# Kernel optimization log

Measured on AMD Instinct MI355X. Metric: run time of the kernel, lower is better.

The kernel has to match this reference:

```python
import jax, jax.numpy as jnp
import numpy as np

N_NODES = 100000
N_EDGES = 1600000
IN_CH = 48
OUT_CH = 64
K = 2


def setup_inputs() -> dict:
    key = jax.random.key(0)
    k1, k2, k3, k4 = jax.random.split(key, 4)
    x = jax.random.normal(k1, (N_NODES, IN_CH), dtype=jnp.float32)
    edge_index = jax.random.randint(k2, (2, N_EDGES), 0, N_NODES, dtype=jnp.int64)
    W = jax.random.normal(k3, (IN_CH, OUT_CH), dtype=jnp.float32) * (1.0 / np.sqrt(IN_CH))
    b = jax.random.normal(k4, (OUT_CH,), dtype=jnp.float32) * 0.01
    return {"x": x, "edge_index": edge_index, "W": W, "b": b}


def _propagate(x, row, col):
    n = x.shape[0]
    # degree of each node counted over col (destination) indices
    deg = jax.ops.segment_sum(jnp.ones_like(col, dtype=x.dtype), col, num_segments=n)
    deg_inv_sqrt = jnp.where(deg > 0, jax.lax.rsqrt(jnp.where(deg > 0, deg, 1.0)), 0.0)
    norm = deg_inv_sqrt[row] * deg_inv_sqrt[col]  # [E]
    # gather-scale-scatter: out[col] += x[row] * norm
    msgs = x[row] * norm[:, None]  # [E, d]
    return jax.ops.segment_sum(msgs, col, num_segments=n)


def reference(x, edge_index, W, b):
    row, col = edge_index[0], edge_index[1]
    h = x
    for _ in range(K):
        h = _propagate(h, row, col)
    return h @ W + b
```

## Files before the change

kernel.cpp:

```cpp
#include <hip/hip_runtime.h>
#include <hip/hip_bf16.h>
#include <hip/hip_fp16.h>


#define N_NODES 100000
#define N_EDGES 1600000
#define IN_CH 48
#define OUT_CH 64
#define NBUCKETS 392
#define CAP 4608
#define EPB 2048
#define EPR 8
#define NBLK_EDGE 782
#define NBLK_BKT 391
#define RSTRIDE 32

__global__ void init_kernel(int* __restrict__ bucketCursor, int* __restrict__ binTotal) {
    int t = threadIdx.x;
    if (t < NBUCKETS) bucketCursor[t] = t * CAP;
    if (t < 64) binTotal[t] = 0;
}

__global__ void bucket_scatter_kernel(const int* __restrict__ row, const int* __restrict__ col,
                                      int* __restrict__ bucketCursor, int* __restrict__ edge_packed) {
    __shared__ int lh[NBUCKETS];
    __shared__ int lofs[NBUCKETS];
    __shared__ int lbase[NBUCKETS];
    __shared__ int stage[EPB];
    __shared__ unsigned short sbkt[EPB];
    __shared__ int wsum[4];
    int tid = threadIdx.x;
    int base = blockIdx.x * EPB;
    for (int i = tid; i < NBUCKETS; i += 256) lh[i] = 0;
    __syncthreads();
    #pragma unroll
    for (int k = 0; k < EPR; k++) {
        int e = base + k * 256 + tid;
        if (e < N_EDGES) atomicAdd(&lh[col[e] >> 8], 1);
    }
    __syncthreads();
    {
        int c0 = (tid < 196) ? lh[2 * tid] : 0;
        int c1 = (tid < 196) ? lh[2 * tid + 1] : 0;
        int s = c0 + c1;
        int incl = s;
        int lane = tid & 63, w = tid >> 6;
        #pragma unroll
        for (int o = 1; o < 64; o <<= 1) {
            int v = __shfl_up(incl, o, 64);
            if (lane >= o) incl += v;
        }
        if (lane == 63) wsum[w] = incl;
        __syncthreads();
        int wbase = 0;
        for (int k = 0; k < w; k++) wbase += wsum[k];
        int ex = wbase + incl - s;
        if (tid < 196) {
            lofs[2 * tid]     = ex;
            lofs[2 * tid + 1] = ex + c0;
        }
    }
    __syncthreads();
    for (int i = tid; i < NBUCKETS; i += 256) {
        int c = lh[i];
        if (c > 0) lbase[i] = atomicAdd(&bucketCursor[i], c);
        lh[i] = 0;
    }
    __syncthreads();
    #pragma unroll
    for (int k = 0; k < EPR; k++) {
        int e = base + k * 256 + tid;
        if (e < N_EDGES) {
            int c = col[e];
            int bkt = c >> 8;
            int r = atomicAdd(&lh[bkt], 1);
            int slot = lofs[bkt] + r;
            stage[slot] = (row[e] << 8) | (c & 255);
            sbkt[slot] = (unsigned short)bkt;
        }
    }
    __syncthreads();
    int total = (base + EPB <= N_EDGES) ? EPB : (N_EDGES - base);
    for (int i = tid; i < total; i += 256) {
        int bkt = sbkt[i];
        int dst = lbase[bkt] + (i - lofs[bkt]);
        if (dst < (bkt + 1) * CAP)
            edge_packed[dst] = stage[i];
    }
}

__global__ void fine_sort_kernel(const int* __restrict__ edge_packed,
                                 const int* __restrict__ bucketCursor,
                                 int* __restrict__ edge_src,
                                 int* __restrict__ deg, int* __restrict__ start,
                                 float* __restrict__ dis, int* __restrict__ binTotal) {
    __shared__ int fh[256];
    __shared__ int cur[256];
    __shared__ int bh[64];
    __shared__ int wsum2[4];
    __shared__ int stage[CAP];
    int b = blockIdx.x;
    int t = threadIdx.x;
    int s0 = b * CAP;
    int s1 = min(bucketCursor[b], (b + 1) * CAP);
    int n_edges = s1 - s0;
    int nodeBase = b << 8;
    if (t < 256) fh[t] = 0;
    if (t < 64) bh[t] = 0;
    __syncthreads();
    for (int j = t; j < n_edges; j += 512) {
        int rc = edge_packed[s0 + j];
        stage[j] = rc;
        atomicAdd(&fh[rc & 255], 1);
    }
    __syncthreads();
    if (t < 256) {
        int c = fh[t];
        int incl = c;
        int sl = t & 63, sw = t >> 6;
        #pragma unroll
        for (int o = 1; o < 64; o <<= 1) {
            int v = __shfl_up(incl, o, 64);
            if (sl >= o) incl += v;
        }
        if (sl == 63) wsum2[sw] = incl;
        __syncthreads();
        int wbase = 0;
        for (int k = 0; k < sw; k++) wbase += wsum2[k];
        incl += wbase;
        int ex = incl - c;
        int node = nodeBase + t;
        bool valid = (node < N_NODES);
        int d = c;
        float dv = (valid && d > 0) ? rsqrtf((float)d) : 0.0f;
        cur[t] = ex;
        if (valid) {
            deg[node] = d;
            start[node] = s0 + ex;
            dis[node] = dv;
            atomicAdd(&bh[min(d, 63)], 1);
        }
    } else {
        __syncthreads();
    }
    __syncthreads();
    for (int j = t; j < n_edges; j += 512) {
        int rc = stage[j];
        int p = atomicAdd(&cur[rc & 255], 1);
        edge_src[s0 + p] = rc >> 8;
    }
    __syncthreads();
    if (t < 64 && bh[t]) atomicAdd(&binTotal[t], bh[t]);
}

__global__ void scale_kernel(const float* __restrict__ x, const float* __restrict__ dis,
                             __half2* __restrict__ xs) {
    int g = blockIdx.x * 32 + (threadIdx.x >> 3);
    int c = (threadIdx.x & 7) * 3;
    float dd = dis[g];
    const float2* px = (const float2*)x + g * 24 + c;
    float2 v0 = px[0], v1 = px[1], v2 = px[2];
    __half2* q = xs + g * RSTRIDE + c;
    q[0] = __floats2half2_rn(v0.x * dd, v0.y * dd);
    q[1] = __floats2half2_rn(v1.x * dd, v1.y * dd);
    q[2] = __floats2half2_rn(v2.x * dd, v2.y * dd);
}

__global__ void binscan_kernel(const int* __restrict__ binTotal, int* __restrict__ binCursor) {
    if (threadIdx.x == 0) {
        int s = 0;
        for (int k = 63; k >= 0; k--) { binCursor[k] = s; s += binTotal[k]; }
    }
}

__global__ void order_kernel(const int* __restrict__ deg, const int* __restrict__ start,
                             const float* __restrict__ dis, int* __restrict__ binCursor,
                             int4* __restrict__ nodeinfo, int n) {
    __shared__ int lhist[64];
    __shared__ int lbase[64];
    int i = blockIdx.x * 256 + threadIdx.x;
    if (threadIdx.x < 64) lhist[threadIdx.x] = 0;
    __syncthreads();
    int bin = 0, myrank = 0;
    if (i < n) {
        bin = min(deg[i], 63);
        myrank = atomicAdd(&lhist[bin], 1);
    }
    __syncthreads();
    if (threadIdx.x < 64 && lhist[threadIdx.x] > 0)
        lbase[threadIdx.x] = atomicAdd(&binCursor[threadIdx.x], lhist[threadIdx.x]);
    __syncthreads();
    if (i < n)
        nodeinfo[lbase[bin] + myrank] = make_int4(i, start[i], deg[i], __float_as_int(dis[i]));
}

#define LOAD3(p, v0, v1, v2) { v0 = (p)[0]; v1 = (p)[1]; v2 = (p)[2]; }
#define ACC6(v0, v1, v2) { \
    float2 u0 = __half22float2(v0), u1 = __half22float2(v1), u2 = __half22float2(v2); \
    a0 += u0.x; a1 += u0.y; a2 += u1.x; a3 += u1.y; a4 += u2.x; a5 += u2.y; }
#define ACC6B(v0, v1, v2) { \
    float2 u0 = __half22float2(v0), u1 = __half22float2(v1), u2 = __half22float2(v2); \
    b0 += u0.x; b1 += u0.y; b2 += u1.x; b3 += u1.y; b4 += u2.x; b5 += u2.y; }

#define DECLD(P) __half2 P##00,P##01,P##02,P##10,P##11,P##12,P##20,P##21,P##22,P##30,P##31,P##32
#define DECLS(S) int S##0, S##1, S##2, S##3
#define LOADSRC(S) { S##0 = edge_src[j]; S##1 = edge_src[j+1]; \
                     S##2 = edge_src[j+2]; S##3 = edge_src[j+3]; j += 4; }
#define ISSUED(P, S, basep) { \
    const __half2* q0 = basep + S##0 * RSTRIDE + lane3; \
    const __half2* q1 = basep + S##1 * RSTRIDE + lane3; \
    const __half2* q2 = basep + S##2 * RSTRIDE + lane3; \
    const __half2* q3 = basep + S##3 * RSTRIDE + lane3; \
    P##00 = q0[0]; P##01 = q0[1]; P##02 = q0[2]; \
    P##10 = q1[0]; P##11 = q1[1]; P##12 = q1[2]; \
    P##20 = q2[0]; P##21 = q2[1]; P##22 = q2[2]; \
    P##30 = q3[0]; P##31 = q3[1]; P##32 = q3[2]; }
#define CONSUMED(P) { ACC6(P##00,P##01,P##02); ACC6B(P##10,P##11,P##12); \
                      ACC6(P##20,P##21,P##22); ACC6B(P##30,P##31,P##32); }

#define GATHER_PIPELINE(basep) { \
    int m = (e - s) >> 2; \
    DECLD(A); DECLD(B); \
    DECLS(sa); DECLS(sb); \
    if (m >= 2) { \
        LOADSRC(sa); LOADSRC(sb); \
        ISSUED(A, sa, basep); \
        m -= 2; \
        while (m >= 2) { \
            LOADSRC(sa); \
            ISSUED(B, sb, basep); \
            CONSUMED(A); \
            LOADSRC(sb); \
            ISSUED(A, sa, basep); \
            CONSUMED(B); \
            m -= 2; \
        } \
        if (m == 1) { \
            LOADSRC(sa); \
            ISSUED(B, sb, basep); \
            CONSUMED(A); \
            ISSUED(A, sa, basep); \
            CONSUMED(B); \
            CONSUMED(A); \
        } else { \
            ISSUED(B, sb, basep); \
            CONSUMED(A); \
            CONSUMED(B); \
        } \
    } else if (m == 1) { \
        LOADSRC(sa); \
        ISSUED(A, sa, basep); \
        CONSUMED(A); \
    } \
    for (; j < e; ++j) { \
        const __half2* p0 = basep + edge_src[j] * RSTRIDE + lane3; \
        __half2 v00, v01, v02; \
        LOAD3(p0, v00, v01, v02); \
        ACC6(v00, v01, v02); \
    } \
    a0 += b0; a1 += b1; a2 += b2; a3 += b3; a4 += b4; a5 += b5; }

__global__ void gather1_kernel(const __half2* __restrict__ xs,
                               const int* __restrict__ edge_src,
                               const int4* __restrict__ nodeinfo,
                               __half2* __restrict__ h1) {
    int g = blockIdx.x * 32 + (threadIdx.x >> 3);
    int lane3 = (threadIdx.x & 7) * 3;
    int4 ni = nodeinfo[g];
    int node = ni.x, s = ni.y, e = s + ni.z;
    float dv = __int_as_float(ni.w);
    float a0 = 0, a1 = 0, a2 = 0, a3 = 0, a4 = 0, a5 = 0;
    float b0 = 0, b1 = 0, b2 = 0, b3 = 0, b4 = 0, b5 = 0;
    int j = s;
    GATHER_PIPELINE(xs);
    float sc = dv * dv;
    __half2* q = h1 + node * RSTRIDE + lane3;
    q[0] = __floats2half2_rn(a0 * sc, a1 * sc);
    q[1] = __floats2half2_rn(a2 * sc, a3 * sc);
    q[2] = __floats2half2_rn(a4 * sc, a5 * sc);
}

__global__ void gather2_gemm_kernel(const __half2* __restrict__ h1,
                                    const int* __restrict__ edge_src,
                                    const int4* __restrict__ nodeinfo,
                                    const float* __restrict__ W,
                                    const float* __restrict__ bias,
                                    float* __restrict__ out) {
    __shared__ float sW[IN_CH * OUT_CH];
    __shared__ float sb[OUT_CH];
    __shared__ float sh[32][IN_CH + 1];

    for (int i = threadIdx.x; i < IN_CH * OUT_CH; i += 256) sW[i] = W[i];
    if (threadIdx.x < OUT_CH) sb[threadIdx.x] = bias[threadIdx.x];

    int nl = threadIdx.x >> 3;
    int lane = threadIdx.x & 7;
    int lane3 = lane * 3;
    int g = blockIdx.x * 32 + nl;
    int4 ni = nodeinfo[g];
    int node = ni.x, s = ni.y, e = s + ni.z;
    float dv = __int_as_float(ni.w);

    float a0 = 0, a1 = 0, a2 = 0, a3 = 0, a4 = 0, a5 = 0;
    float b0 = 0, b1 = 0, b2 = 0, b3 = 0, b4 = 0, b5 = 0;
    int j = s;
    GATHER_PIPELINE(h1);
    int c0 = 6 * lane;
    sh[nl][c0 + 0] = a0 * dv;
    sh[nl][c0 + 1] = a1 * dv;
    sh[nl][c0 + 2] = a2 * dv;
    sh[nl][c0 + 3] = a3 * dv;
    sh[nl][c0 + 4] = a4 * dv;
    sh[nl][c0 + 5] = a5 * dv;
    __syncthreads();

    int j0 = lane * 8;
    float acc[8];
    #pragma unroll
    for (int i = 0; i < 8; i++) acc[i] = sb[j0 + i];
    for (int k = 0; k < IN_CH; k++) {
        float s0 = sh[nl][k];
        #pragma unroll
        for (int i = 0; i < 8; i++) acc[i] += s0 * sW[k * OUT_CH + j0 + i];
    }
    float4* o = (float4*)(out + (size_t)node * OUT_CH + j0);
    o[0] = make_float4(acc[0], acc[1], acc[2], acc[3]);
    o[1] = make_float4(acc[4], acc[5], acc[6], acc[7]);
}

extern "C" void kernel_launch(void* const* d_in, const int* in_sizes, int n_in,
                              void* d_out, int out_size, void* d_ws, size_t ws_size,
                              hipStream_t stream) {
    const float* x   = (const float*)d_in[0];
    const int*   ei  = (const int*)d_in[1];
    const float* W   = (const float*)d_in[2];
    const float* b   = (const float*)d_in[3];
    float* out = (float*)d_out;

    const int* row = ei;
    const int* col = ei + N_EDGES;

    int* ws_i = (int*)d_ws;
    int* bucketCursor = ws_i;
    int* binTotal     = ws_i + 512;
    int* binCursor    = ws_i + 576;
    int* deg          = ws_i + 1024;
    int* start        = ws_i + 101376;
    float* dis        = (float*)(ws_i + 201728);
    int4* nodeinfo    = (int4*)(ws_i + 302080);
    int* edge_packed  = ws_i + 703488;
    __half2* xs       = (__half2*)(ws_i + 703488);
    int* edge_src     = ws_i + 3903488;
    __half2* h1       = (__half2*)(ws_i + 5709824);

    init_kernel<<<1, 512, 0, stream>>>(bucketCursor, binTotal);
    bucket_scatter_kernel<<<NBLK_EDGE, 256, 0, stream>>>(row, col, bucketCursor, edge_packed);
    fine_sort_kernel<<<NBLK_BKT, 512, 0, stream>>>(edge_packed, bucketCursor,
                                                   edge_src, deg, start, dis, binTotal);
    scale_kernel<<<N_NODES / 32, 256, 0, stream>>>(x, dis, xs);
    binscan_kernel<<<1, 64, 0, stream>>>(binTotal, binCursor);
    order_kernel<<<(N_NODES + 255) / 256, 256, 0, stream>>>(deg, start, dis, binCursor,
                                                            nodeinfo, N_NODES);

    gather1_kernel<<<N_NODES / 32, 256, 0, stream>>>(xs, edge_src, nodeinfo, h1);
    gather2_gemm_kernel<<<N_NODES / 32, 256, 0, stream>>>(h1, edge_src, nodeinfo, W, b, out);
}
```

Before: 206.8 us.

## Drop init and binscan kernels, simplify bucket scatter with single pass

```diff
diff --git a/kernel.cpp b/kernel.cpp
--- a/kernel.cpp
+++ b/kernel.cpp
@@ -15,57 +15,15 @@
 #define NBLK_BKT 391
 #define RSTRIDE 32
 
-__global__ void init_kernel(int* __restrict__ bucketCursor, int* __restrict__ binTotal) {
-    int t = threadIdx.x;
-    if (t < NBUCKETS) bucketCursor[t] = t * CAP;
-    if (t < 64) binTotal[t] = 0;
-}
-
 __global__ void bucket_scatter_kernel(const int* __restrict__ row, const int* __restrict__ col,
-                                      int* __restrict__ bucketCursor, int* __restrict__ edge_packed) {
+                                      int* __restrict__ bucketCnt, int* __restrict__ edge_packed) {
     __shared__ int lh[NBUCKETS];
-    __shared__ int lofs[NBUCKETS];
     __shared__ int lbase[NBUCKETS];
-    __shared__ int stage[EPB];
+    __shared__ int rec[EPB];
     __shared__ unsigned short sbkt[EPB];
-    __shared__ int wsum[4];
     int tid = threadIdx.x;
     int base = blockIdx.x * EPB;
     for (int i = tid; i < NBUCKETS; i += 256) lh[i] = 0;
-    __syncthreads();
-    #pragma unroll
-    for (int k = 0; k < EPR; k++) {
-        int e = base + k * 256 + tid;
-        if (e < N_EDGES) atomicAdd(&lh[col[e] >> 8], 1);
-    }
-    __syncthreads();
-    {
-        int c0 = (tid < 196) ? lh[2 * tid] : 0;
-        int c1 = (tid < 196) ? lh[2 * tid + 1] : 0;
-        int s = c0 + c1;
-        int incl = s;
-        int lane = tid & 63, w = tid >> 6;
-        #pragma unroll
-        for (int o = 1; o < 64; o <<= 1) {
-            int v = __shfl_up(incl, o, 64);
-            if (lane >= o) incl += v;
-        }
-        if (lane == 63) wsum[w] = incl;
-        __syncthreads();
-        int wbase = 0;
-        for (int k = 0; k < w; k++) wbase += wsum[k];
-        int ex = wbase + incl - s;
-        if (tid < 196) {
-            lofs[2 * tid]     = ex;
-            lofs[2 * tid + 1] = ex + c0;
-        }
-    }
-    __syncthreads();
-    for (int i = tid; i < NBUCKETS; i += 256) {
-        int c = lh[i];
-        if (c > 0) lbase[i] = atomicAdd(&bucketCursor[i], c);
-        lh[i] = 0;
-    }
     __syncthreads();
     #pragma unroll
     for (int k = 0; k < EPR; k++) {
@@ -73,24 +31,30 @@
         if (e < N_EDGES) {
             int c = col[e];
             int bkt = c >> 8;
-            int r = atomicAdd(&lh[bkt], 1);
-            int slot = lofs[bkt] + r;
-            stage[slot] = (row[e] << 8) | (c & 255);
-            sbkt[slot] = (unsigned short)bkt;
+            rec[k * 256 + tid] = (row[e] << 8) | (c & 255);
+            sbkt[k * 256 + tid] = (unsigned short)bkt;
+            atomicAdd(&lh[bkt], 1);
         }
     }
     __syncthreads();
-    int total = (base + EPB <= N_EDGES) ? EPB : (N_EDGES - base);
+    for (int i = tid; i < NBUCKETS; i += 256) {
+        int c = lh[i];
+        if (c > 0) lbase[i] = i * CAP + atomicAdd(&bucketCnt[i], c);
+        lh[i] = 0;
+    }
+    __syncthreads();
+    int total = min(EPB, N_EDGES - base);
     for (int i = tid; i < total; i += 256) {
         int bkt = sbkt[i];
-        int dst = lbase[bkt] + (i - lofs[bkt]);
+        int p = atomicAdd(&lh[bkt], 1);
+        int dst = lbase[bkt] + p;
         if (dst < (bkt + 1) * CAP)
-            edge_packed[dst] = stage[i];
+            edge_packed[dst] = rec[i];
     }
 }
 
 __global__ void fine_sort_kernel(const int* __restrict__ edge_packed,
-                                 const int* __restrict__ bucketCursor,
+                                 const int* __restrict__ bucketCnt,
                                  int* __restrict__ edge_src,
                                  int* __restrict__ deg, int* __restrict__ start,
                                  float* __restrict__ dis, int* __restrict__ binTotal) {
@@ -102,8 +66,7 @@
     int b = blockIdx.x;
     int t = threadIdx.x;
     int s0 = b * CAP;
-    int s1 = min(bucketCursor[b], (b + 1) * CAP);
-    int n_edges = s1 - s0;
+    int n_edges = min(bucketCnt[b], CAP);
     int nodeBase = b << 8;
     if (t < 256) fh[t] = 0;
     if (t < 64) bh[t] = 0;
@@ -166,32 +129,41 @@
     q[2] = __floats2half2_rn(v2.x * dd, v2.y * dd);
 }
 
-__global__ void binscan_kernel(const int* __restrict__ binTotal, int* __restrict__ binCursor) {
-    if (threadIdx.x == 0) {
-        int s = 0;
-        for (int k = 63; k >= 0; k--) { binCursor[k] = s; s += binTotal[k]; }
-    }
-}
-
 __global__ void order_kernel(const int* __restrict__ deg, const int* __restrict__ start,
-                             const float* __restrict__ dis, int* __restrict__ binCursor,
+                             const float* __restrict__ dis,
+                             const int* __restrict__ binTotal, int* __restrict__ binCursor2,
                              int4* __restrict__ nodeinfo, int n) {
     __shared__ int lhist[64];
     __shared__ int lbase[64];
-    int i = blockIdx.x * 256 + threadIdx.x;
-    if (threadIdx.x < 64) lhist[threadIdx.x] = 0;
-    __syncthreads();
-    int bin = 0, myrank = 0;
+    int t = threadIdx.x;
+    int i = blockIdx.x * 256 + t;
+    if (t < 64) lhist[t] = 0;
+    __syncthreads();
+    int bin = 0, myrank = 0, d = 0;
+    float dv = 0.0f;
     if (i < n) {
-        bin = min(deg[i], 63);
+        d = deg[i];
+        dv = dis[i];
+        bin = min(d, 63);
         myrank = atomicAdd(&lhist[bin], 1);
     }
     __syncthreads();
-    if (threadIdx.x < 64 && lhist[threadIdx.x] > 0)
-        lbase[threadIdx.x] = atomicAdd(&binCursor[threadIdx.x], lhist[threadIdx.x]);
+    if (t < 64) {
+        int c = binTotal[t];
+        int incl = c;
+        #pragma unroll
+        for (int o = 1; o < 64; o <<= 1) {
+            int v = __shfl_up(incl, o, 64);
+            if (t >= o) incl += v;
+        }
+        int tot = __shfl(incl, 63, 64);
+        int S = tot - incl;
+        int add = (lhist[t] > 0) ? atomicAdd(&binCursor2[t], lhist[t]) : 0;
+        lbase[t] = S + add;
+    }
     __syncthreads();
     if (i < n)
-        nodeinfo[lbase[bin] + myrank] = make_int4(i, start[i], deg[i], __float_as_int(dis[i]));
+        nodeinfo[lbase[bin] + myrank] = make_int4(i, start[i], d, __float_as_int(dv));
 }
 
 #define LOAD3(p, v0, v1, v2) { v0 = (p)[0]; v1 = (p)[1]; v2 = (p)[2]; }
@@ -341,9 +313,9 @@
     const int* col = ei + N_EDGES;
 
     int* ws_i = (int*)d_ws;
-    int* bucketCursor = ws_i;
+    int* bucketCnt    = ws_i;
     int* binTotal     = ws_i + 512;
-    int* binCursor    = ws_i + 576;
+    int* binCursor2   = ws_i + 576;
     int* deg          = ws_i + 1024;
     int* start        = ws_i + 101376;
     float* dis        = (float*)(ws_i + 201728);
@@ -353,14 +325,14 @@
     int* edge_src     = ws_i + 3903488;
     __half2* h1       = (__half2*)(ws_i + 5709824);
 
-    init_kernel<<<1, 512, 0, stream>>>(bucketCursor, binTotal);
-    bucket_scatter_kernel<<<NBLK_EDGE, 256, 0, stream>>>(row, col, bucketCursor, edge_packed);
-    fine_sort_kernel<<<NBLK_BKT, 512, 0, stream>>>(edge_packed, bucketCursor,
+    hipMemsetAsync(d_ws, 0, 640 * sizeof(int), stream);
+
+    bucket_scatter_kernel<<<NBLK_EDGE, 256, 0, stream>>>(row, col, bucketCnt, edge_packed);
+    fine_sort_kernel<<<NBLK_BKT, 512, 0, stream>>>(edge_packed, bucketCnt,
                                                    edge_src, deg, start, dis, binTotal);
     scale_kernel<<<N_NODES / 32, 256, 0, stream>>>(x, dis, xs);
-    binscan_kernel<<<1, 64, 0, stream>>>(binTotal, binCursor);
-    order_kernel<<<(N_NODES + 255) / 256, 256, 0, stream>>>(deg, start, dis, binCursor,
-                                                            nodeinfo, N_NODES);
+    order_kernel<<<(N_NODES + 255) / 256, 256, 0, stream>>>(deg, start, dis, binTotal,
+                                                            binCursor2, nodeinfo, N_NODES);
 
     gather1_kernel<<<N_NODES / 32, 256, 0, stream>>>(xs, edge_src, nodeinfo, h1);
     gather2_gemm_kernel<<<N_NODES / 32, 256, 0, stream>>>(h1, edge_src, nodeinfo, W, b, out);
```

New measurement: 206.1 us. Within noise of the previous version (-0.3%).
